# Performance work log

Hardware: AMD Instinct MI355X
Metric: run time of the kernel (lower is better)

Reference implementation:

```python
import jax, jax.numpy as jnp
import numpy as np

B, T, F, H = 1024, 512, 32, 64
EPS = 1e-3  # keras BatchNormalization default epsilon


def lstm_layer(x, Wx, Uh, b):
    """Keras LSTM with activation=relu, recurrent_activation=sigmoid.
    x: [B,T,Fin]; Wx: [Fin,4H]; Uh: [H,4H]; b: [4H]. Gate order i,f,c,o."""
    xz = jnp.einsum('btf,fg->btg', x, Wx) + b  # precompute input projection
    h0 = jnp.zeros((x.shape[0], Uh.shape[0]), x.dtype)

    def step(carry, xz_t):
        h, c = carry
        z = xz_t + h @ Uh
        i, f, g, o = jnp.split(z, 4, axis=-1)
        i = jax.nn.sigmoid(i)
        f = jax.nn.sigmoid(f)
        o = jax.nn.sigmoid(o)
        c = f * c + i * jax.nn.relu(g)
        h = o * jax.nn.relu(c)
        return (h, c), h

    _, hs = jax.lax.scan(step, (h0, h0), jnp.swapaxes(xz, 0, 1))  # [T,B,H]
    return jnp.swapaxes(hs, 0, 1)  # [B,T,H]


def batchnorm(x, gamma, beta, mean, var):
    # inference-mode BN over last axis (keras default axis=-1, training=False)
    return (x - mean) * (gamma * jax.lax.rsqrt(var + EPS)) + beta


def attention(x, W, ht):
    # score = (X @ W) @ h_t -> [B,T]; softmax over time; c_t = X^T @ alpha
    score = jnp.einsum('btd,de,e->bt', x, W, ht[:, 0])
    alpha = jax.nn.softmax(score, axis=1)
    return jnp.einsum('btd,bt->bd', x, alpha)  # [B,H]


def setup_inputs() -> dict:
    key = jax.random.key(0)
    ks = jax.random.split(key, 32)
    d = {'x': jax.random.normal(ks[0], (B, T, F), jnp.float32)}
    fins = [F, H, H]
    for l in range(3):
        fin = fins[l]
        i = l + 1
        d[f'w{i}'] = jax.random.normal(ks[1 + 9 * l], (fin, 4 * H), jnp.float32) * (1.0 / np.sqrt(fin))
        d[f'u{i}'] = jax.random.normal(ks[2 + 9 * l], (H, 4 * H), jnp.float32) * (1.0 / np.sqrt(H))
        d[f'bi{i}'] = jnp.zeros((4 * H,), jnp.float32)
        d[f'gamma{i}'] = jnp.ones((H,), jnp.float32)
        d[f'beta{i}'] = jnp.zeros((H,), jnp.float32)
        d[f'mean{i}'] = jax.random.normal(ks[3 + 9 * l], (H,), jnp.float32) * 0.1
        d[f'var{i}'] = jnp.ones((H,), jnp.float32) + jax.random.uniform(ks[4 + 9 * l], (H,), jnp.float32) * 0.1
        d[f'attw{i}'] = jax.random.truncated_normal(ks[5 + 9 * l], -2, 2, (H, H), jnp.float32) * 0.5
        d[f'attv{i}'] = jax.random.truncated_normal(ks[6 + 9 * l], -2, 2, (H, 1), jnp.float32) * 0.5
    d['dw'] = jax.random.normal(ks[30], (3 * H, 1), jnp.float32) * (1.0 / np.sqrt(3 * H))
    d['db'] = jnp.zeros((1,), jnp.float32)
    return d


def reference(x, w1, u1, bi1, gamma1, beta1, mean1, var1, attw1, attv1,
              w2, u2, bi2, gamma2, beta2, mean2, var2, attw2, attv2,
              w3, u3, bi3, gamma3, beta3, mean3, var3, attw3, attv3,
              dw, db):
    h = lstm_layer(x, w1, u1, bi1)
    h = batchnorm(h, gamma1, beta1, mean1, var1)
    a1 = attention(h, attw1, attv1)
    h = lstm_layer(h, w2, u2, bi2)
    h = batchnorm(h, gamma2, beta2, mean2, var2)
    a2 = attention(h, attw2, attv2)
    h = lstm_layer(h, w3, u3, bi3)
    h = batchnorm(h, gamma3, beta3, mean3, var3)
    a3 = attention(h, attw3, attv3)
    feat = jnp.concatenate([a1, a2, a3], axis=1)  # [B, 3H]
    return feat @ dw + db  # [B, 1]
```

## Files before the change

### kernel.cpp

```cpp
#include <hip/hip_runtime.h>
#include <math.h>

#define BB 1024
#define TT 512
#define FF 32
#define HH 64
#define GG 256
#define TC 64
#define NCHUNK (TT/TC)
#define MB 16
#define NBLK (BB/MB)
#define HPAD 68
#define EPSBN 1e-3f

typedef __attribute__((ext_vector_type(8))) short bf16x8;
typedef __attribute__((ext_vector_type(4))) float f32x4;
typedef __attribute__((ext_vector_type(4))) int   i32x4;
typedef unsigned short ushort_t;

__global__ void fold1_kernel(const float* __restrict__ gamma, const float* __restrict__ beta,
                             const float* __restrict__ mean, const float* __restrict__ var,
                             const float* __restrict__ attw, const float* __restrict__ attv,
                             float* __restrict__ s_out, float* __restrict__ ab_out,
                             float* __restrict__ wv_out) {
    int d = threadIdx.x;
    float s = gamma[d] * rsqrtf(var[d] + EPSBN);
    float ab = beta[d] - mean[d] * s;
    float wvr = 0.f;
    for (int e = 0; e < HH; ++e) wvr += attw[d * HH + e] * attv[e];
    s_out[d] = s;
    ab_out[d] = ab;
    wv_out[d] = s * wvr;
}

__global__ void fold2_kernel(const float* __restrict__ W, const float* __restrict__ b,
                             const float* __restrict__ s_prev, const float* __restrict__ ab_prev,
                             float* __restrict__ Wp, float* __restrict__ bp) {
    int g = threadIdx.x;
    float bacc = b[g];
    for (int d = 0; d < HH; ++d) {
        float w = W[d * GG + g];
        bacc += ab_prev[d] * w;
        Wp[d * GG + g] = s_prev[d] * w;
    }
    bp[g] = bacc;
}

__global__ void init_kernel(float* st_h, float* st_c, float* st_acc, float* st_m, float* st_d) {
    int i = blockIdx.x * blockDim.x + threadIdx.x;
    int n = 3 * BB * HH;
    if (i < n) { st_h[i] = 0.f; st_c[i] = 0.f; st_acc[i] = 0.f; }
    if (i < 3 * BB) { st_m[i] = -3.0e38f; st_d[i] = 0.f; }
}

__device__ __forceinline__ f32x4 ld4(const float* p) { return *reinterpret_cast<const f32x4*>(p); }
__device__ __forceinline__ void st4(float* p, f32x4 v) { *reinterpret_cast<f32x4*>(p) = v; }
__device__ __forceinline__ bf16x8 ldbf(const ushort_t* p) { return *reinterpret_cast<const bf16x8*>(p); }
__device__ __forceinline__ int cvtpk(float a, float b) {
    int r; asm("v_cvt_pk_bf16_f32 %0, %1, %2" : "=v"(r) : "v"(a), "v"(b)); return r;
}
__device__ __forceinline__ void mkfrag(f32x4 A, f32x4 B, bf16x8& hi, bf16x8& lo) {
    i32x4 H, L;
    H[0] = cvtpk(A[0], A[1]); H[1] = cvtpk(A[2], A[3]);
    H[2] = cvtpk(B[0], B[1]); H[3] = cvtpk(B[2], B[3]);
    L[0] = cvtpk(A[0] - __int_as_float(H[0] << 16), A[1] - __int_as_float(H[0] & 0xffff0000));
    L[1] = cvtpk(A[2] - __int_as_float(H[1] << 16), A[3] - __int_as_float(H[1] & 0xffff0000));
    L[2] = cvtpk(B[0] - __int_as_float(H[2] << 16), B[1] - __int_as_float(H[2] & 0xffff0000));
    L[3] = cvtpk(B[2] - __int_as_float(H[3] << 16), B[3] - __int_as_float(H[3] & 0xffff0000));
    hi = __builtin_bit_cast(bf16x8, H); lo = __builtin_bit_cast(bf16x8, L);
}
__device__ __forceinline__ float sigm(float x) { return __fdividef(1.f, 1.f + __expf(-x)); }
#define MFMA(a, b, c) c = __builtin_amdgcn_mfma_f32_16x16x32_bf16(a, b, c, 0, 0, 0)

__global__ void prep_frags(const float* __restrict__ M, int KT, ushort_t* __restrict__ outF) {
    int idx = blockIdx.x * 256 + threadIdx.x;
    int tot = 16 * KT * 512;
    if (idx >= tot) return;
    int e = idx & 7, l = (idx >> 3) & 63, f = idx >> 9;
    int kt = f % KT, gw = f / KT;
    int g = gw & 3, w = gw >> 2;
    int r = l & 15, q = l >> 4;
    int k = 32 * kt + 8 * q + e;
    int col = 64 * g + 16 * w + r;
    float v = M[(size_t)k * GG + col];
    int hb = cvtpk(v, v) & 0xffff;
    float hf = __int_as_float(hb << 16);
    float lo = v - hf;
    int lb = cvtpk(lo, lo) & 0xffff;
    outF[(size_t)(f * 2 + 0) * 512 + l * 8 + e] = (ushort_t)hb;
    outF[(size_t)(f * 2 + 1) * 512 + l * 8 + e] = (ushort_t)lb;
}

__global__ void prep_planes(const float* __restrict__ in, ushort_t* __restrict__ hi,
                            ushort_t* __restrict__ lo, int n4) {
    int i = blockIdx.x * 256 + threadIdx.x;
    if (i >= n4) return;
    f32x4 v = reinterpret_cast<const f32x4*>(in)[i];
    int p0 = cvtpk(v[0], v[1]), p1 = cvtpk(v[2], v[3]);
    float a0 = v[0] - __int_as_float(p0 << 16);
    float a1 = v[1] - __int_as_float(p0 & 0xffff0000);
    float a2 = v[2] - __int_as_float(p1 << 16);
    float a3 = v[3] - __int_as_float(p1 & 0xffff0000);
    int q0 = cvtpk(a0, a1), q1 = cvtpk(a2, a3);
    reinterpret_cast<int2*>(hi)[i] = make_int2(p0, p1);
    reinterpret_cast<int2*>(lo)[i] = make_int2(q0, q1);
}

struct RecFArgs {
    const ushort_t* xhi[3]; const ushort_t* xlo[3]; long sB[3]; long sT[3]; int K[3];
    const ushort_t* UF[3]; const ushort_t* WF[3]; const float* bias[3];
    ushort_t* Hhi[3]; ushort_t* Hlo[3];
    float* st_h[3]; float* st_c[3]; float* st_acc[3];
    float* st_m[3]; float* st_d[3];
    const float* wv[3]; const float* abv[3]; const float* sbn[3];
    float* a_out[3];
    int last[3]; int first[3];
};

template<int KT>
__device__ __forceinline__ void rec_body(const RecFArgs& A, const int seg, const int b0,
                                         float (*hl)[MB][HPAD]) {
    const int tid = threadIdx.x;
    const int w = tid >> 6;
    const int l = tid & 63;
    const int r = l & 15;
    const int q = l >> 4;
    const int cw = w << 4;
    const int grow = b0 + r;

    const bf16x8* UF = reinterpret_cast<const bf16x8*>(A.UF[seg]);
    const bf16x8* WF = reinterpret_cast<const bf16x8*>(A.WF[seg]);
#define LDU(g,kt,p_) UF[(((((w<<2)+(g))*2+(kt))*2)+(p_))*64 + l]
#define LDW(g,kt)    WF[(((((w<<2)+(g))*KT+(kt))*2)+0)*64 + l]
    bf16x8 uh00=LDU(0,0,0), uh01=LDU(0,1,0), uh10=LDU(1,0,0), uh11=LDU(1,1,0),
           uh20=LDU(2,0,0), uh21=LDU(2,1,0), uh30=LDU(3,0,0), uh31=LDU(3,1,0);
    bf16x8 ul00=LDU(0,0,1), ul01=LDU(0,1,1), ul10=LDU(1,0,1), ul11=LDU(1,1,1),
           ul20=LDU(2,0,1), ul21=LDU(2,1,1), ul30=LDU(3,0,1), ul31=LDU(3,1,1);
    bf16x8 wh00=LDW(0,0), wh10=LDW(1,0), wh20=LDW(2,0), wh30=LDW(3,0);
    bf16x8 wh01{}, wh11{}, wh21{}, wh31{};
    if constexpr (KT == 2) {
        wh01=LDW(0,1); wh11=LDW(1,1); wh21=LDW(2,1); wh31=LDW(3,1);
    }

    f32x4 bias40 = ld4(A.bias[seg] +   0 + cw + 4 * q);
    f32x4 bias41 = ld4(A.bias[seg] +  64 + cw + 4 * q);
    f32x4 bias42 = ld4(A.bias[seg] + 128 + cw + 4 * q);
    f32x4 bias43 = ld4(A.bias[seg] + 192 + cw + 4 * q);
    f32x4 wva = ld4(A.wv[seg] + 8 * q);
    f32x4 wvb = ld4(A.wv[seg] + 8 * q + 4);
    f32x4 wvc = ld4(A.wv[seg] + 32 + 8 * q);
    f32x4 wvd = ld4(A.wv[seg] + 32 + 8 * q + 4);

    f32x4 c4   = ld4(A.st_c[seg]   + (size_t)grow * HH + cw + 4 * q);
    f32x4 h4   = ld4(A.st_h[seg]   + (size_t)grow * HH + cw + 4 * q);
    f32x4 acc4 = ld4(A.st_acc[seg] + (size_t)grow * HH + cw + 4 * q);
    float m_b = A.st_m[seg][grow];
    float d_b = A.st_d[seg][grow];

    st4(&hl[0][r][cw + 4 * q], h4);

    const ushort_t* xhib = A.xhi[seg] + (size_t)grow * A.sB[seg];
    const ushort_t* xlob = A.xlo[seg] + (size_t)grow * A.sB[seg];
    const long sT = A.sT[seg];

    bf16x8 xh0 = ldbf(xhib + 8 * q), xl0 = ldbf(xlob + 8 * q);
    bf16x8 xh1{}, xl1{};
    if constexpr (KT == 2) { xh1 = ldbf(xhib + 32 + 8 * q); xl1 = ldbf(xlob + 32 + 8 * q); }
    __syncthreads();

    const bool first = A.first[seg] != 0;
    ushort_t* Hhi = A.Hhi[seg];
    ushort_t* Hlo = A.Hlo[seg];

#pragma unroll 2
    for (int t = 0; t < TC; ++t) {
        const int pr = t & 1;
        f32x4 f0 = ld4(&hl[pr][r][8 * q]);
        f32x4 f1 = ld4(&hl[pr][r][8 * q + 4]);
        f32x4 f2 = ld4(&hl[pr][r][32 + 8 * q]);
        f32x4 f3 = ld4(&hl[pr][r][32 + 8 * q + 4]);
        const int tn = (t + 1 < TC) ? t + 1 : TC - 1;
        const ushort_t* xph = xhib + (size_t)tn * sT + 8 * q;
        const ushort_t* xpl = xlob + (size_t)tn * sT + 8 * q;
        bf16x8 nh0 = ldbf(xph), nl0 = ldbf(xpl), nh1{}, nl1{};
        if constexpr (KT == 2) { nh1 = ldbf(xph + 32); nl1 = ldbf(xpl + 32); }

        f32x4 C0 = bias40, C1 = bias41, C2 = bias42, C3 = bias43;
        MFMA(wh00, xh0, C0); MFMA(wh00, xl0, C0);
        MFMA(wh10, xh0, C1); MFMA(wh10, xl0, C1);
        MFMA(wh20, xh0, C2); MFMA(wh20, xl0, C2);
        MFMA(wh30, xh0, C3); MFMA(wh30, xl0, C3);
        if constexpr (KT == 2) {
            MFMA(wh01, xh1, C0); MFMA(wh01, xl1, C0);
            MFMA(wh11, xh1, C1); MFMA(wh11, xl1, C1);
            MFMA(wh21, xh1, C2); MFMA(wh21, xl1, C2);
            MFMA(wh31, xh1, C3); MFMA(wh31, xl1, C3);
        }

        bf16x8 bh0, bl0, bh1, bl1;
        mkfrag(f0, f1, bh0, bl0);
        mkfrag(f2, f3, bh1, bl1);
        MFMA(uh00, bh0, C0); MFMA(uh00, bl0, C0); MFMA(ul00, bh0, C0);
        MFMA(uh01, bh1, C0); MFMA(uh01, bl1, C0); MFMA(ul01, bh1, C0);
        MFMA(uh10, bh0, C1); MFMA(uh10, bl0, C1); MFMA(ul10, bh0, C1);
        MFMA(uh11, bh1, C1); MFMA(uh11, bl1, C1); MFMA(ul11, bh1, C1);
        MFMA(uh20, bh0, C2); MFMA(uh20, bl0, C2); MFMA(ul20, bh0, C2);
        MFMA(uh21, bh1, C2); MFMA(uh21, bl1, C2); MFMA(ul21, bh1, C2);
        MFMA(uh30, bh0, C3); MFMA(uh30, bl0, C3); MFMA(ul30, bh0, C3);
        MFMA(uh31, bh1, C3); MFMA(uh31, bl1, C3); MFMA(ul31, bh1, C3);

        if (!(first && t == 0)) {
            float sc = 0.f;
#pragma unroll
            for (int i = 0; i < 4; ++i) {
                sc = fmaf(f0[i], wva[i], sc);
                sc = fmaf(f1[i], wvb[i], sc);
                sc = fmaf(f2[i], wvc[i], sc);
                sc = fmaf(f3[i], wvd[i], sc);
            }
            sc += __shfl_xor(sc, 16);
            sc += __shfl_xor(sc, 32);
            float mn = fmaxf(m_b, sc);
            float corr = __expf(m_b - mn);
            float p = __expf(sc - mn);
            d_b = d_b * corr + p;
            acc4 = acc4 * corr + p * h4;
            m_b = mn;
        }

#pragma unroll
        for (int i = 0; i < 4; ++i) {
            float zi = sigm(C0[i]);
            float zf = sigm(C1[i]);
            float zg = fmaxf(C2[i], 0.f);
            float zo = sigm(C3[i]);
            c4[i] = fmaf(zf, c4[i], zi * zg);
            h4[i] = zo * fmaxf(c4[i], 0.f);
        }
        st4(&hl[pr ^ 1][r][cw + 4 * q], h4);
        if (Hhi) {
            int p0 = cvtpk(h4[0], h4[1]), p1 = cvtpk(h4[2], h4[3]);
            float a0 = h4[0] - __int_as_float(p0 << 16);
            float a1 = h4[1] - __int_as_float(p0 & 0xffff0000);
            float a2 = h4[2] - __int_as_float(p1 << 16);
            float a3 = h4[3] - __int_as_float(p1 & 0xffff0000);
            int q0 = cvtpk(a0, a1), q1 = cvtpk(a2, a3);
            size_t ho = (size_t)grow * (TC * HH) + (size_t)t * HH + cw + 4 * q;
            *reinterpret_cast<int2*>(Hhi + ho) = make_int2(p0, p1);
            *reinterpret_cast<int2*>(Hlo + ho) = make_int2(q0, q1);
        }

        xh0 = nh0; xl0 = nl0;
        if constexpr (KT == 2) { xh1 = nh1; xl1 = nl1; }
        __syncthreads();
    }

    if (A.last[seg]) {
        f32x4 f0 = ld4(&hl[0][r][8 * q]);
        f32x4 f1 = ld4(&hl[0][r][8 * q + 4]);
        f32x4 f2 = ld4(&hl[0][r][32 + 8 * q]);
        f32x4 f3 = ld4(&hl[0][r][32 + 8 * q + 4]);
        float sc = 0.f;
#pragma unroll
        for (int i = 0; i < 4; ++i) {
            sc = fmaf(f0[i], wva[i], sc);
            sc = fmaf(f1[i], wvb[i], sc);
            sc = fmaf(f2[i], wvc[i], sc);
            sc = fmaf(f3[i], wvd[i], sc);
        }
        sc += __shfl_xor(sc, 16);
        sc += __shfl_xor(sc, 32);
        float mn = fmaxf(m_b, sc);
        float corr = __expf(m_b - mn);
        float p = __expf(sc - mn);
        d_b = d_b * corr + p;
        acc4 = acc4 * corr + p * h4;
        m_b = mn;
        f32x4 sb = ld4(A.sbn[seg] + cw + 4 * q);
        f32x4 ab = ld4(A.abv[seg] + cw + 4 * q);
        f32x4 res;
#pragma unroll
        for (int i = 0; i < 4; ++i)
            res[i] = sb[i] * __fdividef(acc4[i], d_b) + ab[i];
        st4(A.a_out[seg] + (size_t)grow * HH + cw + 4 * q, res);
    }
    st4(A.st_c[seg]   + (size_t)grow * HH + cw + 4 * q, c4);
    st4(A.st_h[seg]   + (size_t)grow * HH + cw + 4 * q, h4);
    st4(A.st_acc[seg] + (size_t)grow * HH + cw + 4 * q, acc4);
    if (w == 0 && q == 0) { A.st_m[seg][grow] = m_b; A.st_d[seg][grow] = d_b; }
#undef LDU
#undef LDW
}

__global__ __launch_bounds__(256, 2) void rec_mfma(RecFArgs A) {
    __shared__ float hl[2][MB][HPAD];
    const int seg = blockIdx.x >> 6;
    const int b0 = (blockIdx.x & (NBLK - 1)) << 4;
    if (A.K[seg] == 32) rec_body<1>(A, seg, b0, hl);
    else                rec_body<2>(A, seg, b0, hl);
}

__global__ void final_kernel(const float* __restrict__ a, const float* __restrict__ dw,
                             const float* __restrict__ db, float* __restrict__ out) {
    int b = blockIdx.x * blockDim.x + threadIdx.x;
    if (b >= BB) return;
    float acc = db[0];
    for (int l = 0; l < 3; ++l)
        for (int j = 0; j < HH; ++j)
            acc += a[(l * BB + b) * HH + j] * dw[l * HH + j];
    out[b] = acc;
}

extern "C" void kernel_launch(void* const* d_in, const int* in_sizes, int n_in,
                              void* d_out, int out_size, void* d_ws, size_t ws_size,
                              hipStream_t stream) {
    (void)in_sizes; (void)n_in; (void)out_size; (void)ws_size;
    const float* x = (const float*)d_in[0];
    const float* w[3]    = {(const float*)d_in[1],  (const float*)d_in[10], (const float*)d_in[19]};
    const float* uu[3]   = {(const float*)d_in[2],  (const float*)d_in[11], (const float*)d_in[20]};
    const float* bi[3]   = {(const float*)d_in[3],  (const float*)d_in[12], (const float*)d_in[21]};
    const float* gam[3]  = {(const float*)d_in[4],  (const float*)d_in[13], (const float*)d_in[22]};
    const float* bet[3]  = {(const float*)d_in[5],  (const float*)d_in[14], (const float*)d_in[23]};
    const float* mea[3]  = {(const float*)d_in[6],  (const float*)d_in[15], (const float*)d_in[24]};
    const float* var[3]  = {(const float*)d_in[7],  (const float*)d_in[16], (const float*)d_in[25]};
    const float* atw[3]  = {(const float*)d_in[8],  (const float*)d_in[17], (const float*)d_in[26]};
    const float* atv[3]  = {(const float*)d_in[9],  (const float*)d_in[18], (const float*)d_in[27]};
    const float* dw = (const float*)d_in[28];
    const float* db = (const float*)d_in[29];

    float* ws = (float*)d_ws;
    size_t off = 0;
    ushort_t* Hhi[2][2]; ushort_t* Hlo[2][2];
    for (int l = 0; l < 2; ++l)
        for (int p = 0; p < 2; ++p) {
            Hhi[l][p] = (ushort_t*)(ws + off); off += (size_t)BB * TC * HH / 2;
            Hlo[l][p] = (ushort_t*)(ws + off); off += (size_t)BB * TC * HH / 2;
        }
    ushort_t* Xhi = (ushort_t*)(ws + off); off += (size_t)BB * TT * FF / 2;
    ushort_t* Xlo = (ushort_t*)(ws + off); off += (size_t)BB * TT * FF / 2;
    float* st_h  = ws + off; off += 3 * BB * HH;
    float* st_c  = ws + off; off += 3 * BB * HH;
    float* st_ac = ws + off; off += 3 * BB * HH;
    float* st_m  = ws + off; off += 3 * BB;
    float* st_d  = ws + off; off += 3 * BB;
    float* s_ws  = ws + off; off += 3 * HH;
    float* ab_ws = ws + off; off += 3 * HH;
    float* wv_ws = ws + off; off += 3 * HH;
    float* W2p   = ws + off; off += HH * GG;
    float* W3p   = ws + off; off += HH * GG;
    float* b2p   = ws + off; off += GG;
    float* b3p   = ws + off; off += GG;
    float* a_ws  = ws + off; off += 3 * BB * HH;
    ushort_t* UFb[3]; ushort_t* WFb[3];
    for (int l = 0; l < 3; ++l) { UFb[l] = (ushort_t*)(ws + off); off += 16384; }
    for (int l = 0; l < 3; ++l) { WFb[l] = (ushort_t*)(ws + off); off += 16384; }

    for (int l = 0; l < 3; ++l)
        fold1_kernel<<<1, 64, 0, stream>>>(gam[l], bet[l], mea[l], var[l], atw[l], atv[l],
                                           s_ws + l * HH, ab_ws + l * HH, wv_ws + l * HH);
    fold2_kernel<<<1, 256, 0, stream>>>(w[1], bi[1], s_ws + 0 * HH, ab_ws + 0 * HH, W2p, b2p);
    fold2_kernel<<<1, 256, 0, stream>>>(w[2], bi[2], s_ws + 1 * HH, ab_ws + 1 * HH, W3p, b3p);
    init_kernel<<<(3 * BB * HH + 255) / 256, 256, 0, stream>>>(st_h, st_c, st_ac, st_m, st_d);

    for (int l = 0; l < 3; ++l)
        prep_frags<<<64, 256, 0, stream>>>(uu[l], 2, UFb[l]);
    prep_frags<<<32, 256, 0, stream>>>(w[0], 1, WFb[0]);
    prep_frags<<<64, 256, 0, stream>>>(W2p, 2, WFb[1]);
    prep_frags<<<64, 256, 0, stream>>>(W3p, 2, WFb[2]);
    {
        int n4 = BB * TT * FF / 4;
        prep_planes<<<(n4 + 255) / 256, 256, 0, stream>>>(x, Xhi, Xlo, n4);
    }

    const float* bl[3] = {bi[0], b2p, b3p};

    for (int s = 0; s <= NCHUNK - 1 + 2; ++s) {
        RecFArgs ra;
        int nseg = 0;
        for (int l = 0; l < 3; ++l) {
            int cpos = s - l;
            if (cpos < 0 || cpos >= NCHUNK) continue;
            if (l == 0) {
                ra.xhi[nseg] = Xhi + (size_t)cpos * TC * FF;
                ra.xlo[nseg] = Xlo + (size_t)cpos * TC * FF;
                ra.sB[nseg] = (long)TT * FF;
                ra.sT[nseg] = FF;
                ra.K[nseg] = 32;
            } else {
                int par = (s & 1) ^ 1;
                ra.xhi[nseg] = Hhi[l - 1][par];
                ra.xlo[nseg] = Hlo[l - 1][par];
                ra.sB[nseg] = (long)TC * HH;
                ra.sT[nseg] = HH;
                ra.K[nseg] = 64;
            }
            ra.UF[nseg] = UFb[l]; ra.WF[nseg] = WFb[l]; ra.bias[nseg] = bl[l];
            ra.Hhi[nseg] = (l < 2) ? Hhi[l][s & 1] : (ushort_t*)0;
            ra.Hlo[nseg] = (l < 2) ? Hlo[l][s & 1] : (ushort_t*)0;
            ra.st_h[nseg] = st_h + l * BB * HH;
            ra.st_c[nseg] = st_c + l * BB * HH;
            ra.st_acc[nseg] = st_ac + l * BB * HH;
            ra.st_m[nseg] = st_m + l * BB;
            ra.st_d[nseg] = st_d + l * BB;
            ra.wv[nseg]  = wv_ws + l * HH;
            ra.abv[nseg] = ab_ws + l * HH;
            ra.sbn[nseg] = s_ws + l * HH;
            ra.a_out[nseg] = a_ws + l * BB * HH;
            ra.last[nseg]  = (cpos == NCHUNK - 1) ? 1 : 0;
            ra.first[nseg] = (cpos == 0) ? 1 : 0;
            ++nseg;
        }
        if (!nseg) continue;
        rec_mfma<<<nseg * NBLK, 256, 0, stream>>>(ra);
    }
    final_kernel<<<(BB + 255) / 256, 256, 0, stream>>>(a_ws, dw, db, (float*)d_out);
}
```

Measured before the change: 819.0 us.

## Pack two 16-row batch groups per 512-thread block and add W low-part MFMAs

The recurrence kernel now launches 512-thread blocks, each holding two independent 16-row batch groups with separate shared-memory h buffers. This halves the grid size and changes launch bounds from (256,2) to (512,1), to amortise per-block overhead and share weight fetches on a CU. It also adds the bf16 low-part W fragments to the input projection, giving a three-term split product like the U path. That extra term costs more MFMA work per step in exchange for accuracy. With fewer blocks, far fewer CUs may be busy in this latency-bound recurrence.

After: 1.259 ms. 1.54x slower.

```diff
diff --git a/kernel.cpp b/kernel.cpp
--- a/kernel.cpp
+++ b/kernel.cpp
@@ -9,7 +9,7 @@
 #define TC 64
 #define NCHUNK (TT/TC)
 #define MB 16
-#define NBLK (BB/MB)
+#define NBLK2 32
 #define HPAD 68
 #define EPSBN 1e-3f
 
@@ -119,8 +119,7 @@
 
 template<int KT>
 __device__ __forceinline__ void rec_body(const RecFArgs& A, const int seg, const int b0,
-                                         float (*hl)[MB][HPAD]) {
-    const int tid = threadIdx.x;
+                                         const int tid, float (*hl)[MB][HPAD]) {
     const int w = tid >> 6;
     const int l = tid & 63;
     const int r = l & 15;
@@ -131,15 +130,17 @@
     const bf16x8* UF = reinterpret_cast<const bf16x8*>(A.UF[seg]);
     const bf16x8* WF = reinterpret_cast<const bf16x8*>(A.WF[seg]);
 #define LDU(g,kt,p_) UF[(((((w<<2)+(g))*2+(kt))*2)+(p_))*64 + l]
-#define LDW(g,kt)    WF[(((((w<<2)+(g))*KT+(kt))*2)+0)*64 + l]
+#define LDW(g,kt,p_) WF[(((((w<<2)+(g))*KT+(kt))*2)+(p_))*64 + l]
     bf16x8 uh00=LDU(0,0,0), uh01=LDU(0,1,0), uh10=LDU(1,0,0), uh11=LDU(1,1,0),
            uh20=LDU(2,0,0), uh21=LDU(2,1,0), uh30=LDU(3,0,0), uh31=LDU(3,1,0);
     bf16x8 ul00=LDU(0,0,1), ul01=LDU(0,1,1), ul10=LDU(1,0,1), ul11=LDU(1,1,1),
            ul20=LDU(2,0,1), ul21=LDU(2,1,1), ul30=LDU(3,0,1), ul31=LDU(3,1,1);
-    bf16x8 wh00=LDW(0,0), wh10=LDW(1,0), wh20=LDW(2,0), wh30=LDW(3,0);
-    bf16x8 wh01{}, wh11{}, wh21{}, wh31{};
+    bf16x8 wh00=LDW(0,0,0), wh10=LDW(1,0,0), wh20=LDW(2,0,0), wh30=LDW(3,0,0);
+    bf16x8 wl00=LDW(0,0,1), wl10=LDW(1,0,1), wl20=LDW(2,0,1), wl30=LDW(3,0,1);
+    bf16x8 wh01{}, wh11{}, wh21{}, wh31{}, wl01{}, wl11{}, wl21{}, wl31{};
     if constexpr (KT == 2) {
-        wh01=LDW(0,1); wh11=LDW(1,1); wh21=LDW(2,1); wh31=LDW(3,1);
+        wh01=LDW(0,1,0); wh11=LDW(1,1,0); wh21=LDW(2,1,0); wh31=LDW(3,1,0);
+        wl01=LDW(0,1,1); wl11=LDW(1,1,1); wl21=LDW(2,1,1); wl31=LDW(3,1,1);
     }
 
     f32x4 bias40 = ld4(A.bias[seg] +   0 + cw + 4 * q);
@@ -186,15 +187,15 @@
         if constexpr (KT == 2) { nh1 = ldbf(xph + 32); nl1 = ldbf(xpl + 32); }
 
         f32x4 C0 = bias40, C1 = bias41, C2 = bias42, C3 = bias43;
-        MFMA(wh00, xh0, C0); MFMA(wh00, xl0, C0);
-        MFMA(wh10, xh0, C1); MFMA(wh10, xl0, C1);
-        MFMA(wh20, xh0, C2); MFMA(wh20, xl0, C2);
-        MFMA(wh30, xh0, C3); MFMA(wh30, xl0, C3);
+        MFMA(wh00, xh0, C0); MFMA(wh00, xl0, C0); MFMA(wl00, xh0, C0);
+        MFMA(wh10, xh0, C1); MFMA(wh10, xl0, C1); MFMA(wl10, xh0, C1);
+        MFMA(wh20, xh0, C2); MFMA(wh20, xl0, C2); MFMA(wl20, xh0, C2);
+        MFMA(wh30, xh0, C3); MFMA(wh30, xl0, C3); MFMA(wl30, xh0, C3);
         if constexpr (KT == 2) {
-            MFMA(wh01, xh1, C0); MFMA(wh01, xl1, C0);
-            MFMA(wh11, xh1, C1); MFMA(wh11, xl1, C1);
-            MFMA(wh21, xh1, C2); MFMA(wh21, xl1, C2);
-            MFMA(wh31, xh1, C3); MFMA(wh31, xl1, C3);
+            MFMA(wh01, xh1, C0); MFMA(wh01, xl1, C0); MFMA(wl01, xh1, C0);
+            MFMA(wh11, xh1, C1); MFMA(wh11, xl1, C1); MFMA(wl11, xh1, C1);
+            MFMA(wh21, xh1, C2); MFMA(wh21, xl1, C2); MFMA(wl21, xh1, C2);
+            MFMA(wh31, xh1, C3); MFMA(wh31, xl1, C3); MFMA(wl31, xh1, C3);
         }
 
         bf16x8 bh0, bl0, bh1, bl1;
@@ -292,12 +293,14 @@
 #undef LDW
 }
 
-__global__ __launch_bounds__(256, 2) void rec_mfma(RecFArgs A) {
-    __shared__ float hl[2][MB][HPAD];
-    const int seg = blockIdx.x >> 6;
-    const int b0 = (blockIdx.x & (NBLK - 1)) << 4;
-    if (A.K[seg] == 32) rec_body<1>(A, seg, b0, hl);
-    else                rec_body<2>(A, seg, b0, hl);
+__global__ __launch_bounds__(512, 1) void rec_mfma(RecFArgs A) {
+    __shared__ float hl[2][2][MB][HPAD];
+    const int seg = blockIdx.x >> 5;
+    const int grp = threadIdx.x >> 8;
+    const int b0 = ((blockIdx.x & (NBLK2 - 1)) << 5) + (grp << 4);
+    const int tid = threadIdx.x & 255;
+    if (A.K[seg] == 32) rec_body<1>(A, seg, b0, tid, hl[grp]);
+    else                rec_body<2>(A, seg, b0, tid, hl[grp]);
 }
 
 __global__ void final_kernel(const float* __restrict__ a, const float* __restrict__ dw,
@@ -411,7 +414,7 @@
             ++nseg;
         }
         if (!nseg) continue;
-        rec_mfma<<<nseg * NBLK, 256, 0, stream>>>(ra);
+        rec_mfma<<<nseg * NBLK2, 512, 0, stream>>>(ra);
     }
     final_kernel<<<(BB + 255) / 256, 256, 0, stream>>>(a_ws, dw, db, (float*)d_out);
 }
```
